# Performance work log

Hardware: AMD Instinct MI355X
Metric: run time of the kernel (lower is better)

The kernel has to match this reference:

```python
import jax, jax.numpy as jnp
import numpy as np

N = 300000  # active lattice vertices
K = 9       # permutohedral 1-ring stencil: center + 2*(d+1) neighbors, d=3
F = 64      # nr_filters


def setup_inputs() -> dict:
    key = jax.random.key(0)
    k1, k2, k3, k4 = jax.random.split(key, 4)
    lv = jax.random.normal(k1, (N, F), dtype=jnp.float32)
    neighbors = jax.random.randint(k2, (N, K), 0, N, dtype=jnp.int64)
    # center tap is the vertex itself (tap 0)
    neighbors = neighbors.at[:, 0].set(jnp.arange(N, dtype=jnp.int64))
    scale = 1.0 / np.sqrt(K * F)
    w1 = jax.random.normal(k3, (K, F, F), dtype=jnp.float32) * scale
    w2 = jax.random.normal(k4, (K, F, F), dtype=jnp.float32) * scale
    b1 = jnp.zeros((F,), dtype=jnp.float32)
    b2 = jnp.zeros((F,), dtype=jnp.float32)
    return {"lv": lv, "neighbors": neighbors, "w1": w1, "b1": b1, "w2": w2, "b2": b2}


def _lattice_conv(x, neighbors, w, b):
    # gather neighbor values: [N, K, F], then per-tap matmul and sum over taps
    g = x[neighbors]  # irregular gather
    return jnp.einsum('nkf,kfo->no', g, w) + b


def reference(lv, neighbors, w1, b1, w2, b2):
    identity = lv
    # ReluConv 1: relu -> lattice conv (dropout disabled)
    x = _lattice_conv(jax.nn.relu(lv), neighbors, w1, b1)
    # ReluConv 2: relu -> lattice conv
    x = _lattice_conv(jax.nn.relu(x), neighbors, w2, b2)
    # residual add
    return x + identity
```

## Files before the change

kernel.cpp:

```cpp
#include <hip/hip_runtime.h>

#define NV 300000
#define KT 9
#define NF 64
#define NBLK ((NV + 63) / 64)

typedef __attribute__((ext_vector_type(8))) short bf16x8;
typedef __attribute__((ext_vector_type(4))) float f32x4;
typedef __attribute__((ext_vector_type(4))) float f4;
typedef __attribute__((ext_vector_type(4))) unsigned short u16x4;

__device__ __forceinline__ unsigned short f2bf(float f) {
    union { float f; unsigned int u; } a; a.f = f;
    unsigned int u = a.u;
    return (unsigned short)((u + 0x7FFFu + ((u >> 16) & 1u)) >> 16);
}

__global__ void prep_kernel(const float* __restrict__ lv,
                            const float* __restrict__ w1,
                            const float* __restrict__ w2,
                            unsigned short* __restrict__ xbf0,
                            unsigned short* __restrict__ wt1,
                            unsigned short* __restrict__ wt2) {
    int b = blockIdx.x;
    if (b < 18) {
        const float* w = (b < 9) ? w1 : w2;
        unsigned short* wt = (b < 9) ? wt1 : wt2;
        int k = (b < 9) ? b : b - 9;
        for (int e = threadIdx.x; e < NF * NF; e += 256) {
            int o = e >> 6, f = e & 63;
            wt[(k * NF + o) * NF + f] = f2bf(w[(k * NF + f) * NF + o]);
        }
    } else {
        const int n4 = NV * NF / 4;
        int i = (b - 18) * 256 + threadIdx.x;
        if (i < n4) {
            f4 v = ((const f4*)lv)[i];
            u16x4 r;
            #pragma unroll
            for (int j = 0; j < 4; ++j) r[j] = f2bf(fmaxf(v[j], 0.f));
            ((u16x4*)xbf0)[i] = r;
        }
    }
}

template<int LAYER>
__global__ __launch_bounds__(256, 4)
void conv_kernel(const unsigned short* __restrict__ xin,
                 const int* __restrict__ nbr,
                 const unsigned short* __restrict__ wt,
                 const float* __restrict__ bias,
                 const float* __restrict__ resid,
                 unsigned short* __restrict__ bfout,
                 float* __restrict__ fout)
{
    __shared__ unsigned short gA[4][64][64];
    __shared__ int nbs[576];

    const int tid  = threadIdx.x;
    const int lane = tid & 63;
    const int wv   = tid >> 6;
    const int base = blockIdx.x * 64;

    for (int e = tid; e < 576; e += 256) {
        long ge = (long)base * 9 + e;
        nbs[e] = (ge < (long)NV * 9) ? nbr[ge] : 0;
    }

    const int bcol = wv * 16 + (lane & 15);
    const int bk   = (lane >> 4) * 8;
    bf16x8 bw[KT][2];
    #pragma unroll
    for (int k = 0; k < KT; ++k) {
        #pragma unroll
        for (int kk = 0; kk < 2; ++kk)
            bw[k][kk] = *(const bf16x8*)&wt[(k * 64 + bcol) * 64 + kk * 32 + bk];
    }

    f32x4 acc[4];
    #pragma unroll
    for (int im = 0; im < 4; ++im) acc[im] = (f32x4){0.f, 0.f, 0.f, 0.f};

    __syncthreads();

    const int sr_off = lane >> 3;
    const int sj     = lane & 7;
    auto stage = [&](int k) {
        #pragma unroll
        for (int h = 0; h < 2; ++h) {
            const int rblk = wv + h * 4;
            const int r    = rblk * 8 + sr_off;
            const int nb   = nbs[r * 9 + k];
            const int gcol = sj ^ (r & 7);
            const unsigned short* src = xin + nb * 64 + gcol * 8;
            __builtin_amdgcn_global_load_lds(
                (const __attribute__((address_space(1))) unsigned int*)src,
                (__attribute__((address_space(3))) unsigned int*)&gA[k & 3][rblk * 8][0],
                16, 0, 0);
        }
    };

    auto tap = [&](int k) {
        #pragma unroll
        for (int im = 0; im < 4; ++im) {
            #pragma unroll
            for (int kk = 0; kk < 2; ++kk) {
                const int row = im * 16 + (lane & 15);
                const int c16 = kk * 4 + (lane >> 4);
                const int swc = c16 ^ (row & 7);
                bf16x8 a = *(const bf16x8*)&gA[k & 3][row][swc * 8];
                acc[im] = __builtin_amdgcn_mfma_f32_16x16x32_bf16(a, bw[k][kk], acc[im], 0, 0, 0);
            }
        }
    };

    stage(0); stage(1); stage(2);

    #define PHASE(K, VM, DO_STAGE)                                    \
        asm volatile("s_waitcnt vmcnt(" #VM ")" ::: "memory");        \
        __builtin_amdgcn_s_barrier();                                 \
        if (DO_STAGE) stage((K) + 3);                                 \
        tap(K);
    PHASE(0, 4, 1) PHASE(1, 4, 1) PHASE(2, 4, 1) PHASE(3, 4, 1)
    PHASE(4, 4, 1) PHASE(5, 4, 1) PHASE(6, 4, 0) PHASE(7, 2, 0)
    PHASE(8, 0, 0)
    #undef PHASE

    const int ocol = wv * 16 + (lane & 15);
    const int orow = (lane >> 4) * 4;
    const float bv = bias[ocol];
    #pragma unroll
    for (int im = 0; im < 4; ++im) {
        #pragma unroll
        for (int j = 0; j < 4; ++j) {
            const int r = base + im * 16 + orow + j;
            if (r < NV) {
                float v = acc[im][j] + bv;
                if (LAYER == 1) {
                    bfout[r * 64 + ocol] = f2bf(fmaxf(v, 0.f));
                } else {
                    fout[r * 64 + ocol] = v + resid[r * 64 + ocol];
                }
            }
        }
    }
}

extern "C" void kernel_launch(void* const* d_in, const int* in_sizes, int n_in,
                              void* d_out, int out_size, void* d_ws, size_t ws_size,
                              hipStream_t stream) {
    const float* lv  = (const float*)d_in[0];
    const int*   nbr = (const int*)d_in[1];
    const float* w1  = (const float*)d_in[2];
    const float* b1  = (const float*)d_in[3];
    const float* w2  = (const float*)d_in[4];
    const float* b2  = (const float*)d_in[5];
    float* out = (float*)d_out;

    char* ws = (char*)d_ws;
    unsigned short* xbf0 = (unsigned short*)ws;
    unsigned short* xbf1 = (unsigned short*)(ws + 38400000);
    unsigned short* wt1  = (unsigned short*)(ws + 76800000);
    unsigned short* wt2  = (unsigned short*)(ws + 76873728);

    const int n4blk = (NV * NF / 4 + 255) / 256;
    prep_kernel<<<18 + n4blk, 256, 0, stream>>>(lv, w1, w2, xbf0, wt1, wt2);
    conv_kernel<1><<<NBLK, 256, 0, stream>>>(xbf0, nbr, wt1, b1, nullptr, xbf1, nullptr);
    conv_kernel<2><<<NBLK, 256, 0, stream>>>(xbf1, nbr, wt2, b2, lv, nullptr, out);
}
```

Before: 316.4 us.

## Double-buffer gather staging and stream weights per tap to raise occupancy

Cuts the LDS gather ring from four buffers to two and stops preloading all nine taps of weights into registers. Weights for each tap are now loaded just ahead of use, into a two-slot register buffer. This frees registers and LDS so the launch bound can target 8 waves instead of 4, giving more memory-level parallelism for the irregular gather. In exchange the prefetch depth drops from three taps to two, each phase gains an extra barrier, and weights are re-read from cache on every tap.

```diff
diff --git a/kernel.cpp b/kernel.cpp
--- a/kernel.cpp
+++ b/kernel.cpp
@@ -45,7 +45,7 @@
 }
 
 template<int LAYER>
-__global__ __launch_bounds__(256, 4)
+__global__ __launch_bounds__(256, 8)
 void conv_kernel(const unsigned short* __restrict__ xin,
                  const int* __restrict__ nbr,
                  const unsigned short* __restrict__ wt,
@@ -54,7 +54,7 @@
                  unsigned short* __restrict__ bfout,
                  float* __restrict__ fout)
 {
-    __shared__ unsigned short gA[4][64][64];
+    __shared__ unsigned short gA[2][64][64];
     __shared__ int nbs[576];
 
     const int tid  = threadIdx.x;
@@ -69,13 +69,9 @@
 
     const int bcol = wv * 16 + (lane & 15);
     const int bk   = (lane >> 4) * 8;
-    bf16x8 bw[KT][2];
-    #pragma unroll
-    for (int k = 0; k < KT; ++k) {
-        #pragma unroll
-        for (int kk = 0; kk < 2; ++kk)
-            bw[k][kk] = *(const bf16x8*)&wt[(k * 64 + bcol) * 64 + kk * 32 + bk];
-    }
+    auto ldw = [&](int k, int kk) {
+        return *(const bf16x8*)&wt[(k * 64 + bcol) * 64 + kk * 32 + bk];
+    };
 
     f32x4 acc[4];
     #pragma unroll
@@ -95,12 +91,12 @@
             const unsigned short* src = xin + nb * 64 + gcol * 8;
             __builtin_amdgcn_global_load_lds(
                 (const __attribute__((address_space(1))) unsigned int*)src,
-                (__attribute__((address_space(3))) unsigned int*)&gA[k & 3][rblk * 8][0],
+                (__attribute__((address_space(3))) unsigned int*)&gA[k & 1][rblk * 8][0],
                 16, 0, 0);
         }
     };
 
-    auto tap = [&](int k) {
+    auto tap = [&](int k, bf16x8 (&bwk)[2]) {
         #pragma unroll
         for (int im = 0; im < 4; ++im) {
             #pragma unroll
@@ -108,23 +104,35 @@
                 const int row = im * 16 + (lane & 15);
                 const int c16 = kk * 4 + (lane >> 4);
                 const int swc = c16 ^ (row & 7);
-                bf16x8 a = *(const bf16x8*)&gA[k & 3][row][swc * 8];
-                acc[im] = __builtin_amdgcn_mfma_f32_16x16x32_bf16(a, bw[k][kk], acc[im], 0, 0, 0);
+                bf16x8 a = *(const bf16x8*)&gA[k & 1][row][swc * 8];
+                acc[im] = __builtin_amdgcn_mfma_f32_16x16x32_bf16(a, bwk[kk], acc[im], 0, 0, 0);
             }
         }
     };
 
-    stage(0); stage(1); stage(2);
+    #define FENCE asm volatile("" ::: "memory")
 
-    #define PHASE(K, VM, DO_STAGE)                                    \
-        asm volatile("s_waitcnt vmcnt(" #VM ")" ::: "memory");        \
-        __builtin_amdgcn_s_barrier();                                 \
-        if (DO_STAGE) stage((K) + 3);                                 \
-        tap(K);
-    PHASE(0, 4, 1) PHASE(1, 4, 1) PHASE(2, 4, 1) PHASE(3, 4, 1)
-    PHASE(4, 4, 1) PHASE(5, 4, 1) PHASE(6, 4, 0) PHASE(7, 2, 0)
-    PHASE(8, 0, 0)
+    bf16x8 bwreg[2][2];
+
+    bwreg[0][0] = ldw(0, 0); bwreg[0][1] = ldw(0, 1); stage(0); FENCE;
+    bwreg[1][0] = ldw(1, 0); bwreg[1][1] = ldw(1, 1); stage(1); FENCE;
+
+    #define PHASE(K, VM)                                                   \
+        asm volatile("s_waitcnt vmcnt(" #VM ")" ::: "memory");             \
+        __builtin_amdgcn_s_barrier();                                      \
+        tap(K, bwreg[(K) & 1]);                                            \
+        FENCE;                                                             \
+        __builtin_amdgcn_s_barrier();                                      \
+        if ((K) + 2 <= 8) {                                                \
+            stage((K) + 2);                                                \
+            bwreg[(K) & 1][0] = ldw((K) + 2, 0);                           \
+            bwreg[(K) & 1][1] = ldw((K) + 2, 1);                           \
+        }                                                                  \
+        FENCE;
+    PHASE(0, 4) PHASE(1, 4) PHASE(2, 4) PHASE(3, 4) PHASE(4, 4)
+    PHASE(5, 4) PHASE(6, 4) PHASE(7, 4) PHASE(8, 0)
     #undef PHASE
+    #undef FENCE
 
     const int ocol = wv * 16 + (lane & 15);
     const int orow = (lane >> 4) * 4;
```

Result: faster. 282.3 us (-10.8%).
